# Kernel optimization log

Hardware: AMD Instinct MI355X
Metric: run time of the kernel (lower is better)

## Reference

```python
import jax, jax.numpy as jnp
import numpy as np

B, H, S, D = 2, 16, 2048, 64

def setup_inputs() -> dict:
    key = jax.random.key(0)
    kq, kk, kv = jax.random.split(key, 3)
    Q = jax.random.normal(kq, (B, H, S, D), dtype=jnp.float32)
    K = jax.random.normal(kk, (B, H, S, D), dtype=jnp.float32)
    V = jax.random.normal(kv, (B, H, S, D), dtype=jnp.float32)
    return {"Q": Q, "K": K, "V": V}

def reference(Q, K, V):
    scale = 1.0 / jnp.sqrt(jnp.asarray(Q.shape[-1], dtype=Q.dtype))
    # [B,H,S,S] scores, scaled post-matmul to match torch source
    scores = jnp.einsum('bhqd,bhkd->bhqk', Q, K) * scale
    attn = jax.nn.softmax(scores, axis=-1)
    return jnp.einsum('bhqk,bhkd->bhqd', attn, V)
```

## Files before the change

kernel.cpp:

```cpp
#include <hip/hip_runtime.h>

typedef __bf16 bf16;
typedef __bf16 bf16x4 __attribute__((ext_vector_type(4)));
typedef __bf16 bf16x8 __attribute__((ext_vector_type(8)));
typedef float  f32x4  __attribute__((ext_vector_type(4)));

#define S_LEN 2048
#define DHEAD 64
#define BH    32
#define QB    128
#define KB    64
#define NT    (S_LEN / KB)

static __device__ __forceinline__ void async_cp16(const bf16* g, bf16* l) {
  __builtin_amdgcn_global_load_lds(
      (const __attribute__((address_space(1))) void*)g,
      (__attribute__((address_space(3))) void*)l, 16, 0, 0);
}

static __device__ __forceinline__ f32x4 mfma_bf16(bf16x8 a, bf16x8 b, f32x4 c) {
  return __builtin_amdgcn_mfma_f32_16x16x32_bf16(a, b, c, 0, 0, 0);
}

__global__ __launch_bounds__(256)
void kv_prep(const float* __restrict__ K, const float* __restrict__ V,
             bf16* __restrict__ Kb, bf16* __restrict__ Vt) {
  __shared__ bf16 t[64][72];
  const int bh = blockIdx.x >> 5;
  const int kt = blockIdx.x & 31;
  const int tid = threadIdx.x;
  const size_t tbase = ((size_t)bh * S_LEN + kt * 64) * DHEAD;

  const float* ksrc = K + tbase;
  bf16* kdst = Kb + tbase;
#pragma unroll
  for (int it = 0; it < 2; ++it) {
    const int i = tid + it * 256;
    const float4 a = ((const float4*)ksrc)[2 * i];
    const float4 b = ((const float4*)ksrc)[2 * i + 1];
    bf16x8 o;
    o[0] = (bf16)a.x; o[1] = (bf16)a.y; o[2] = (bf16)a.z; o[3] = (bf16)a.w;
    o[4] = (bf16)b.x; o[5] = (bf16)b.y; o[6] = (bf16)b.z; o[7] = (bf16)b.w;
    ((bf16x8*)kdst)[i] = o;
  }

  const float* vsrc = V + tbase;
  bf16* vdst = Vt + (size_t)bh * DHEAD * S_LEN + kt * 64;
#pragma unroll
  for (int it = 0; it < 4; ++it) {
    const int i = tid + it * 256;
    const int r = i >> 4, c4 = (i & 15) << 2;
    const float4 v = *(const float4*)(vsrc + (size_t)r * DHEAD + c4);
    bf16x4 o;
    o[0] = (bf16)v.x; o[1] = (bf16)v.y; o[2] = (bf16)v.z; o[3] = (bf16)v.w;
    *(bf16x4*)&t[r][c4] = o;
  }
  __syncthreads();
#pragma unroll
  for (int it = 0; it < 2; ++it) {
    const int j = tid + it * 256;
    const int d = j >> 3, c8 = (j & 7) << 3;
    bf16x8 o;
#pragma unroll
    for (int e = 0; e < 8; ++e) o[e] = t[c8 + e][d];
    *(bf16x8*)(vdst + (size_t)d * S_LEN + c8) = o;
  }
}

__global__ __launch_bounds__(256, 2)
void attn_fwd5(const float* __restrict__ Qg0, const bf16* __restrict__ Kb0,
               const bf16* __restrict__ Vt0, float* __restrict__ Og0) {
  __shared__ __align__(16) bf16 Kl[2][KB * DHEAD];
  __shared__ __align__(16) bf16 Vl[2][DHEAD * KB];
  __shared__ __align__(16) bf16 Pl[4][32][64];

  const int tid = threadIdx.x, wid = tid >> 6, lane = tid & 63;
  const int l15 = lane & 15, lg = lane >> 4;
  const int bh = blockIdx.x >> 4;
  const int qb = blockIdx.x & 15;
  const int qbase = qb * QB + wid * 32;

  const float* Qg = Qg0 + (size_t)bh * S_LEN * DHEAD;
  const bf16* Kb = Kb0 + (size_t)bh * S_LEN * DHEAD;
  const bf16* Vt = Vt0 + (size_t)bh * DHEAD * S_LEN;
  float* Og = Og0 + (size_t)bh * S_LEN * DHEAD;

  const int srow = wid * 8 + (lane >> 3);
  const int scl = ((lane & 7) ^ (srow & 7)) << 3;
  const bf16* kg0 = Kb + (size_t)srow * DHEAD + scl;
  const bf16* vg0 = Vt + (size_t)srow * S_LEN + scl;

#define STAGE(b, t)                                                  \
  do {                                                               \
    const bf16* kg_ = kg0 + (size_t)(t) * KB * DHEAD;                \
    const bf16* vg_ = vg0 + (t) * KB;                                \
    async_cp16(kg_, &Kl[b][wid * 512]);                              \
    async_cp16(kg_ + 32 * DHEAD, &Kl[b][2048 + wid * 512]);          \
    async_cp16(vg_, &Vl[b][wid * 512]);                              \
    async_cp16(vg_ + (size_t)32 * S_LEN, &Vl[b][2048 + wid * 512]);  \
  } while (0)

  const float qscale = 0.125f * 1.44269504088896341f;
  bf16x8 qfrag[2][2];
#pragma unroll
  for (int rs = 0; rs < 2; ++rs) {
    const float* qrow = Qg + (size_t)(qbase + rs * 16 + l15) * DHEAD;
#pragma unroll
    for (int h = 0; h < 2; ++h) {
      const float* p = qrow + h * 32 + lg * 8;
      const float4 a = *(const float4*)(p);
      const float4 b = *(const float4*)(p + 4);
      bf16x8 f;
      f[0] = (bf16)(a.x * qscale); f[1] = (bf16)(a.y * qscale);
      f[2] = (bf16)(a.z * qscale); f[3] = (bf16)(a.w * qscale);
      f[4] = (bf16)(b.x * qscale); f[5] = (bf16)(b.y * qscale);
      f[6] = (bf16)(b.z * qscale); f[7] = (bf16)(b.w * qscale);
      qfrag[rs][h] = f;
    }
  }

  float m_l[2] = {-__builtin_inff(), -__builtin_inff()};
  float l_l[2] = {0.f, 0.f};
  f32x4 o_acc[2][4];
#pragma unroll
  for (int rs = 0; rs < 2; ++rs)
#pragma unroll
    for (int nd = 0; nd < 4; ++nd) o_acc[rs][nd] = f32x4{0.f, 0.f, 0.f, 0.f};

  const int kxor = (l15 & 7) << 4;
  const int pswz = (l15 & 7) << 4;
  char* pbase0 = (char*)&Pl[wid][0][0] + l15 * 128;
  char* pbase1 = pbase0 + 16 * 128;

  STAGE(0, 0);
  __syncthreads();

  for (int kt = 0; kt < NT; ++kt) {
    const int cur = kt & 1;
    if (kt + 1 < NT) STAGE(cur ^ 1, kt + 1);

    f32x4 sacc[2][4] = {};
    __builtin_amdgcn_s_setprio(1);
#pragma unroll
    for (int ns = 0; ns < 4; ++ns) {
      const int krow = ns * 16 + l15;
#pragma unroll
      for (int h = 0; h < 2; ++h) {
        const int kb = krow * 128 + ((((h << 2) + lg) << 4) ^ kxor);
        const bf16x8 kf = *(const bf16x8*)((const char*)&Kl[cur][0] + kb);
        sacc[0][ns] = mfma_bf16(kf, qfrag[0][h], sacc[0][ns]);
        sacc[1][ns] = mfma_bf16(kf, qfrag[1][h], sacc[1][ns]);
      }
    }
    __builtin_amdgcn_s_setprio(0);

#pragma unroll
    for (int rs = 0; rs < 2; ++rs) {
      float pmax = sacc[rs][0][0];
#pragma unroll
      for (int ns = 0; ns < 4; ++ns)
#pragma unroll
        for (int r = 0; r < 4; ++r) pmax = fmaxf(pmax, sacc[rs][ns][r]);

      if (!__all(pmax <= m_l[rs] + 8.f)) {
        pmax = fmaxf(pmax, __shfl_xor(pmax, 16));
        pmax = fmaxf(pmax, __shfl_xor(pmax, 32));
        const float mn = fmaxf(m_l[rs], pmax);
        const float alpha = __builtin_amdgcn_exp2f(m_l[rs] - mn);
        m_l[rs] = mn;
        l_l[rs] *= alpha;
#pragma unroll
        for (int r = 0; r < 4; ++r) {
          const float a_r = __shfl(alpha, (lane & 48) | (((lane >> 4) & 3) * 4 + r));
          o_acc[rs][0][r] *= a_r;
          o_acc[rs][1][r] *= a_r;
          o_acc[rs][2][r] *= a_r;
          o_acc[rs][3][r] *= a_r;
        }
      }

      char* pb = rs ? pbase1 : pbase0;
      float rsum = 0.f;
#pragma unroll
      for (int ns = 0; ns < 4; ++ns) {
#pragma unroll
        for (int r = 0; r < 4; ++r) {
          const float p = __builtin_amdgcn_exp2f(sacc[rs][ns][r] - m_l[rs]);
          sacc[rs][ns][r] = p;
          rsum += p;
        }
        bf16x4 pw;
        pw[0] = (bf16)sacc[rs][ns][0]; pw[1] = (bf16)sacc[rs][ns][1];
        pw[2] = (bf16)sacc[rs][ns][2]; pw[3] = (bf16)sacc[rs][ns][3];
        *(bf16x4*)(pb + (((ns << 5) + (lg << 3)) ^ pswz)) = pw;
      }
      l_l[rs] += rsum;
    }

    asm volatile("s_waitcnt lgkmcnt(0)" ::: "memory");

    __builtin_amdgcn_s_setprio(1);
#pragma unroll
    for (int h = 0; h < 2; ++h) {
      const int poff = ((h << 6) + (lg << 4)) ^ pswz;
      const bf16x8 pf0 = *(const bf16x8*)(pbase0 + poff);
      const bf16x8 pf1 = *(const bf16x8*)(pbase1 + poff);
#pragma unroll
      for (int nd = 0; nd < 4; ++nd) {
        const int vrow = nd * 16 + l15;
        const int vb = vrow * 128 + ((((h << 2) + lg) << 4) ^ kxor);
        const bf16x8 vf = *(const bf16x8*)((const char*)&Vl[cur][0] + vb);
        o_acc[0][nd] = mfma_bf16(pf0, vf, o_acc[0][nd]);
        o_acc[1][nd] = mfma_bf16(pf1, vf, o_acc[1][nd]);
      }
    }
    __builtin_amdgcn_s_setprio(0);
    __syncthreads();
  }

#pragma unroll
  for (int rs = 0; rs < 2; ++rs) {
    l_l[rs] += __shfl_xor(l_l[rs], 16);
    l_l[rs] += __shfl_xor(l_l[rs], 32);
#pragma unroll
    for (int r = 0; r < 4; ++r) {
      const float l_r = __shfl(l_l[rs], (lane & 48) | (((lane >> 4) & 3) * 4 + r));
      const float inv = 1.0f / l_r;
      float* orow = Og + (size_t)(qbase + rs * 16 + lg * 4 + r) * DHEAD;
#pragma unroll
      for (int nd = 0; nd < 4; ++nd)
        orow[nd * 16 + l15] = o_acc[rs][nd][r] * inv;
    }
  }
#undef STAGE
}

__global__ __launch_bounds__(256, 2)
void attn_fb(const float* __restrict__ Qg0, const float* __restrict__ Kg0,
             const float* __restrict__ Vg0, float* __restrict__ Og0) {
  __shared__ __align__(16) bf16 Kl[KB][72];
  __shared__ __align__(16) bf16 Vt[DHEAD][72];
  __shared__ __align__(16) bf16 Pl[4][16][72];
  const int tid = threadIdx.x, wid = tid >> 6, lane = tid & 63;
  const int l15 = lane & 15, lg = lane >> 4;
  const int bh = blockIdx.x >> 5, qb = blockIdx.x & 31;
  const int qbase = qb * 64 + wid * 16;
  const size_t base = (size_t)bh * S_LEN * DHEAD;
  const float* Qg = Qg0 + base;
  const float* Kg = Kg0 + base;
  const float* Vg = Vg0 + base;
  float* Og = Og0 + base;
  const float qscale = 0.125f * 1.44269504088896341f;
  bf16x8 qfrag[2];
  {
    const float* qrow = Qg + (size_t)(qbase + l15) * DHEAD;
#pragma unroll
    for (int h = 0; h < 2; ++h) {
      const float* p = qrow + h * 32 + lg * 8;
      const float4 a = *(const float4*)(p);
      const float4 b = *(const float4*)(p + 4);
      bf16x8 f;
      f[0] = (bf16)(a.x * qscale); f[1] = (bf16)(a.y * qscale);
      f[2] = (bf16)(a.z * qscale); f[3] = (bf16)(a.w * qscale);
      f[4] = (bf16)(b.x * qscale); f[5] = (bf16)(b.y * qscale);
      f[6] = (bf16)(b.z * qscale); f[7] = (bf16)(b.w * qscale);
      qfrag[h] = f;
    }
  }
  float m_r[4], l_r[4];
  f32x4 o_acc[4];
#pragma unroll
  for (int r = 0; r < 4; ++r) {
    m_r[r] = -__builtin_inff();
    l_r[r] = 0.f;
    o_acc[r] = f32x4{0.f, 0.f, 0.f, 0.f};
  }
  for (int kt = 0; kt < NT; ++kt) {
    __syncthreads();
#pragma unroll
    for (int it = 0; it < 4; ++it) {
      const int i = tid + it * 256;
      const int row = i >> 4, c4 = (i & 15) << 2;
      const float4 kk = *(const float4*)(Kg + (size_t)(kt * KB + row) * DHEAD + c4);
      bf16x4 kb;
      kb[0] = (bf16)kk.x; kb[1] = (bf16)kk.y; kb[2] = (bf16)kk.z; kb[3] = (bf16)kk.w;
      *(bf16x4*)&Kl[row][c4] = kb;
      const float4 vv = *(const float4*)(Vg + (size_t)(kt * KB + row) * DHEAD + c4);
      Vt[c4 + 0][row] = (bf16)vv.x;
      Vt[c4 + 1][row] = (bf16)vv.y;
      Vt[c4 + 2][row] = (bf16)vv.z;
      Vt[c4 + 3][row] = (bf16)vv.w;
    }
    __syncthreads();
    f32x4 sacc[4] = {};
#pragma unroll
    for (int ns = 0; ns < 4; ++ns)
#pragma unroll
      for (int h = 0; h < 2; ++h) {
        const bf16x8 kf = *(const bf16x8*)&Kl[ns * 16 + l15][h * 32 + lg * 8];
        sacc[ns] = mfma_bf16(qfrag[h], kf, sacc[ns]);
      }
    float rmax[4], alpha[4], rsum[4];
#pragma unroll
    for (int r = 0; r < 4; ++r)
      rmax[r] = fmaxf(fmaxf(sacc[0][r], sacc[1][r]), fmaxf(sacc[2][r], sacc[3][r]));
#pragma unroll
    for (int off = 1; off < 16; off <<= 1)
#pragma unroll
      for (int r = 0; r < 4; ++r)
        rmax[r] = fmaxf(rmax[r], __shfl_xor(rmax[r], off));
#pragma unroll
    for (int r = 0; r < 4; ++r) {
      const float mn = fmaxf(m_r[r], rmax[r]);
      alpha[r] = exp2f(m_r[r] - mn);
      m_r[r] = mn;
      rsum[r] = 0.f;
    }
#pragma unroll
    for (int ns = 0; ns < 4; ++ns)
#pragma unroll
      for (int r = 0; r < 4; ++r) {
        const float p = exp2f(sacc[ns][r] - m_r[r]);
        sacc[ns][r] = p;
        rsum[r] += p;
      }
#pragma unroll
    for (int off = 1; off < 16; off <<= 1)
#pragma unroll
      for (int r = 0; r < 4; ++r)
        rsum[r] += __shfl_xor(rsum[r], off);
#pragma unroll
    for (int r = 0; r < 4; ++r) {
      l_r[r] = l_r[r] * alpha[r] + rsum[r];
      o_acc[0][r] *= alpha[r];
      o_acc[1][r] *= alpha[r];
      o_acc[2][r] *= alpha[r];
      o_acc[3][r] *= alpha[r];
    }
#pragma unroll
    for (int ns = 0; ns < 4; ++ns)
#pragma unroll
      for (int r = 0; r < 4; ++r)
        Pl[wid][lg * 4 + r][ns * 16 + l15] = (bf16)sacc[ns][r];
    asm volatile("s_waitcnt lgkmcnt(0)" ::: "memory");
#pragma unroll
    for (int h = 0; h < 2; ++h) {
      const bf16x8 pf = *(const bf16x8*)&Pl[wid][l15][h * 32 + lg * 8];
#pragma unroll
      for (int nd = 0; nd < 4; ++nd) {
        const bf16x8 vf = *(const bf16x8*)&Vt[nd * 16 + l15][h * 32 + lg * 8];
        o_acc[nd] = mfma_bf16(pf, vf, o_acc[nd]);
      }
    }
  }
#pragma unroll
  for (int r = 0; r < 4; ++r) {
    const float inv = 1.0f / l_r[r];
    float* orow = Og + (size_t)(qbase + lg * 4 + r) * DHEAD;
#pragma unroll
    for (int nd = 0; nd < 4; ++nd)
      orow[nd * 16 + l15] = o_acc[nd][r] * inv;
  }
}

extern "C" void kernel_launch(void* const* d_in, const int* in_sizes, int n_in,
                              void* d_out, int out_size, void* d_ws, size_t ws_size,
                              hipStream_t stream) {
  const float* Q = (const float*)d_in[0];
  const float* K = (const float*)d_in[1];
  const float* V = (const float*)d_in[2];
  float* O = (float*)d_out;

  const size_t elems = (size_t)BH * S_LEN * DHEAD;
  const size_t bf16_bytes = elems * 2;
  if (ws_size >= 2 * bf16_bytes) {
    bf16* Kb = (bf16*)d_ws;
    bf16* Vt = (bf16*)((char*)d_ws + bf16_bytes);
    hipLaunchKernelGGL(kv_prep, dim3(BH * 32), dim3(256), 0, stream, K, V, Kb, Vt);
    hipLaunchKernelGGL(attn_fwd5, dim3(BH * (S_LEN / QB)), dim3(256), 0, stream,
                       Q, Kb, Vt, O);
  } else {
    hipLaunchKernelGGL(attn_fb, dim3(1024), dim3(256), 0, stream, Q, K, V, O);
  }
}
```

Baseline: 141.9 us.

## Keep P in registers and load V directly in MFMA fragment layout

The prep kernel now writes V pre-swizzled into the exact per-lane MFMA B-operand fragment order. The attention kernel then loads V fragments straight from global memory into registers, with no LDS staging. P is repacked in registers into the A-operand layout instead of going through an LDS round trip, which removes the P shared buffer and the lgkmcnt wait. The block index is also swizzled to group blocks across heads for L2 locality. The trade-off is more global loads per wave each iteration, with 16 waves reading the same V tile, no async prefetch for V, and higher register pressure.

```diff
diff --git a/kernel.cpp b/kernel.cpp
--- a/kernel.cpp
+++ b/kernel.cpp
@@ -23,8 +23,8 @@
 }
 
 __global__ __launch_bounds__(256)
-void kv_prep(const float* __restrict__ K, const float* __restrict__ V,
-             bf16* __restrict__ Kb, bf16* __restrict__ Vt) {
+void kv_prep2(const float* __restrict__ K, const float* __restrict__ V,
+              bf16* __restrict__ Kb, bf16* __restrict__ Vf) {
   __shared__ bf16 t[64][72];
   const int bh = blockIdx.x >> 5;
   const int kt = blockIdx.x & 31;
@@ -45,7 +45,6 @@
   }
 
   const float* vsrc = V + tbase;
-  bf16* vdst = Vt + (size_t)bh * DHEAD * S_LEN + kt * 64;
 #pragma unroll
   for (int it = 0; it < 4; ++it) {
     const int i = tid + it * 256;
@@ -56,48 +55,47 @@
     *(bf16x4*)&t[r][c4] = o;
   }
   __syncthreads();
-#pragma unroll
-  for (int it = 0; it < 2; ++it) {
-    const int j = tid + it * 256;
-    const int d = j >> 3, c8 = (j & 7) << 3;
+
+  bf16* vdst = Vf + (size_t)bh * S_LEN * DHEAD + (size_t)kt * 4096;
+  const int lane = tid & 63, nd = tid >> 6;
+  const int lg = lane >> 4, l15 = lane & 15;
+#pragma unroll
+  for (int h = 0; h < 2; ++h) {
     bf16x8 o;
 #pragma unroll
-    for (int e = 0; e < 8; ++e) o[e] = t[c8 + e][d];
-    *(bf16x8*)(vdst + (size_t)d * S_LEN + c8) = o;
+    for (int j = 0; j < 8; ++j)
+      o[j] = t[32 * h + 16 * (j >> 2) + 4 * lg + (j & 3)][nd * 16 + l15];
+    *(bf16x8*)(vdst + ((nd * 2 + h) * 64 + lane) * 8) = o;
   }
 }
 
 __global__ __launch_bounds__(256, 2)
-void attn_fwd5(const float* __restrict__ Qg0, const bf16* __restrict__ Kb0,
-               const bf16* __restrict__ Vt0, float* __restrict__ Og0) {
+void attn_fwd6(const float* __restrict__ Qg0, const bf16* __restrict__ Kb0,
+               const bf16* __restrict__ Vf0, float* __restrict__ Og0) {
   __shared__ __align__(16) bf16 Kl[2][KB * DHEAD];
-  __shared__ __align__(16) bf16 Vl[2][DHEAD * KB];
-  __shared__ __align__(16) bf16 Pl[4][32][64];
 
   const int tid = threadIdx.x, wid = tid >> 6, lane = tid & 63;
   const int l15 = lane & 15, lg = lane >> 4;
-  const int bh = blockIdx.x >> 4;
-  const int qb = blockIdx.x & 15;
+  const int bid = blockIdx.x;
+  const int swz = ((bid & 7) << 6) | (bid >> 3);
+  const int bh = swz >> 4;
+  const int qb = swz & 15;
   const int qbase = qb * QB + wid * 32;
 
   const float* Qg = Qg0 + (size_t)bh * S_LEN * DHEAD;
   const bf16* Kb = Kb0 + (size_t)bh * S_LEN * DHEAD;
-  const bf16* Vt = Vt0 + (size_t)bh * DHEAD * S_LEN;
+  const bf16* Vf = Vf0 + (size_t)bh * S_LEN * DHEAD;
   float* Og = Og0 + (size_t)bh * S_LEN * DHEAD;
 
   const int srow = wid * 8 + (lane >> 3);
   const int scl = ((lane & 7) ^ (srow & 7)) << 3;
   const bf16* kg0 = Kb + (size_t)srow * DHEAD + scl;
-  const bf16* vg0 = Vt + (size_t)srow * S_LEN + scl;
-
-#define STAGE(b, t)                                                  \
-  do {                                                               \
-    const bf16* kg_ = kg0 + (size_t)(t) * KB * DHEAD;                \
-    const bf16* vg_ = vg0 + (t) * KB;                                \
-    async_cp16(kg_, &Kl[b][wid * 512]);                              \
-    async_cp16(kg_ + 32 * DHEAD, &Kl[b][2048 + wid * 512]);          \
-    async_cp16(vg_, &Vl[b][wid * 512]);                              \
-    async_cp16(vg_ + (size_t)32 * S_LEN, &Vl[b][2048 + wid * 512]);  \
+
+#define STAGE(b, t)                                            \
+  do {                                                         \
+    const bf16* kg_ = kg0 + (size_t)(t) * KB * DHEAD;          \
+    async_cp16(kg_, &Kl[b][wid * 512]);                        \
+    async_cp16(kg_ + 32 * DHEAD, &Kl[b][2048 + wid * 512]);    \
   } while (0)
 
   const float qscale = 0.125f * 1.44269504088896341f;
@@ -128,9 +126,7 @@
     for (int nd = 0; nd < 4; ++nd) o_acc[rs][nd] = f32x4{0.f, 0.f, 0.f, 0.f};
 
   const int kxor = (l15 & 7) << 4;
-  const int pswz = (l15 & 7) << 4;
-  char* pbase0 = (char*)&Pl[wid][0][0] + l15 * 128;
-  char* pbase1 = pbase0 + 16 * 128;
+  const bf16* vlane = Vf + lane * 8;
 
   STAGE(0, 0);
   __syncthreads();
@@ -138,6 +134,16 @@
   for (int kt = 0; kt < NT; ++kt) {
     const int cur = kt & 1;
     if (kt + 1 < NT) STAGE(cur ^ 1, kt + 1);
+
+    bf16x8 vf[2][4];
+    {
+      const bf16* vb = vlane + (size_t)kt * 4096;
+#pragma unroll
+      for (int nd = 0; nd < 4; ++nd)
+#pragma unroll
+        for (int h = 0; h < 2; ++h)
+          vf[h][nd] = *(const bf16x8*)(vb + (nd * 2 + h) * 512);
+    }
 
     f32x4 sacc[2][4] = {};
     __builtin_amdgcn_s_setprio(1);
@@ -154,6 +160,7 @@
     }
     __builtin_amdgcn_s_setprio(0);
 
+    bf16x8 pa[2][2];
 #pragma unroll
     for (int rs = 0; rs < 2; ++rs) {
       float pmax = sacc[rs][0][0];
@@ -179,41 +186,37 @@
         }
       }
 
-      char* pb = rs ? pbase1 : pbase0;
       float rsum = 0.f;
 #pragma unroll
-      for (int ns = 0; ns < 4; ++ns) {
+      for (int ns = 0; ns < 4; ++ns)
 #pragma unroll
         for (int r = 0; r < 4; ++r) {
           const float p = __builtin_amdgcn_exp2f(sacc[rs][ns][r] - m_l[rs]);
           sacc[rs][ns][r] = p;
           rsum += p;
         }
-        bf16x4 pw;
-        pw[0] = (bf16)sacc[rs][ns][0]; pw[1] = (bf16)sacc[rs][ns][1];
-        pw[2] = (bf16)sacc[rs][ns][2]; pw[3] = (bf16)sacc[rs][ns][3];
-        *(bf16x4*)(pb + (((ns << 5) + (lg << 3)) ^ pswz)) = pw;
-      }
       l_l[rs] += rsum;
-    }
-
-    asm volatile("s_waitcnt lgkmcnt(0)" ::: "memory");
+
+      bf16x8 w0, w1;
+#pragma unroll
+      for (int r = 0; r < 4; ++r) {
+        w0[r]     = (bf16)sacc[rs][0][r];
+        w0[r + 4] = (bf16)sacc[rs][1][r];
+        w1[r]     = (bf16)sacc[rs][2][r];
+        w1[r + 4] = (bf16)sacc[rs][3][r];
+      }
+      pa[rs][0] = w0;
+      pa[rs][1] = w1;
+    }
 
     __builtin_amdgcn_s_setprio(1);
 #pragma unroll
-    for (int h = 0; h < 2; ++h) {
-      const int poff = ((h << 6) + (lg << 4)) ^ pswz;
-      const bf16x8 pf0 = *(const bf16x8*)(pbase0 + poff);
-      const bf16x8 pf1 = *(const bf16x8*)(pbase1 + poff);
+    for (int h = 0; h < 2; ++h)
 #pragma unroll
       for (int nd = 0; nd < 4; ++nd) {
-        const int vrow = nd * 16 + l15;
-        const int vb = vrow * 128 + ((((h << 2) + lg) << 4) ^ kxor);
-        const bf16x8 vf = *(const bf16x8*)((const char*)&Vl[cur][0] + vb);
-        o_acc[0][nd] = mfma_bf16(pf0, vf, o_acc[0][nd]);
-        o_acc[1][nd] = mfma_bf16(pf1, vf, o_acc[1][nd]);
-      }
-    }
+        o_acc[0][nd] = mfma_bf16(pa[0][h], vf[h][nd], o_acc[0][nd]);
+        o_acc[1][nd] = mfma_bf16(pa[1][h], vf[h][nd], o_acc[1][nd]);
+      }
     __builtin_amdgcn_s_setprio(0);
     __syncthreads();
   }
@@ -375,10 +378,10 @@
   const size_t bf16_bytes = elems * 2;
   if (ws_size >= 2 * bf16_bytes) {
     bf16* Kb = (bf16*)d_ws;
-    bf16* Vt = (bf16*)((char*)d_ws + bf16_bytes);
-    hipLaunchKernelGGL(kv_prep, dim3(BH * 32), dim3(256), 0, stream, K, V, Kb, Vt);
-    hipLaunchKernelGGL(attn_fwd5, dim3(BH * (S_LEN / QB)), dim3(256), 0, stream,
-                       Q, Kb, Vt, O);
+    bf16* Vf = (bf16*)((char*)d_ws + bf16_bytes);
+    hipLaunchKernelGGL(kv_prep2, dim3(BH * 32), dim3(256), 0, stream, K, V, Kb, Vf);
+    hipLaunchKernelGGL(attn_fwd6, dim3(BH * (S_LEN / QB)), dim3(256), 0, stream,
+                       Q, Kb, Vf, O);
   } else {
     hipLaunchKernelGGL(attn_fb, dim3(1024), dim3(256), 0, stream, Q, K, V, O);
   }
```

New measurement: 135.2 us. -4.7%, faster.
